# Kernel optimization log

Measured on AMD Instinct MI355X. Metric: run time of the kernel, lower is better.

The kernel has to match this reference:

```python
import jax, jax.numpy as jnp
import numpy as np

G = 64          # groups of the dynamic conv
EPS = 1e-5      # instance-norm epsilon


def setup_inputs() -> dict:
    key = jax.random.key(0)
    ks = jax.random.split(key, 12)
    B, Cin, Cout, S = 16, 512, 256, 512   # batch, in_ch, out_ch, style_dim
    H = W = 32
    cg = Cin // G                          # channels per group (= 8)

    def n(k, shape, scale=0.05):
        return jax.random.normal(k, shape, dtype=jnp.float32) * scale

    return {
        "x": jax.random.normal(ks[0], (B, Cin, H, W), dtype=jnp.float32),
        "w": jax.random.normal(ks[1], (B, S, 3, 3), dtype=jnp.float32),
        # KernelPredictor params
        "kp_sw": n(ks[2], (Cin * cg, S, 3, 3)),   # spatial (depthwise) kernel predictor conv
        "kp_sb": n(ks[3], (Cin * cg,)),
        "kp_pw": n(ks[4], (Cin * cg, S)),          # pointwise kernel predictor (1x1 on pooled style)
        "kp_pb": n(ks[5], (Cin * cg,)),
        "kp_bw": n(ks[6], (Cin, S)),               # bias predictor
        "kp_bb": n(ks[7], (Cin,)),
        # decoder conv stack (convs=2, last changes channels)
        "dec_w1": n(ks[8], (Cin, Cin, 3, 3)),
        "dec_b1": n(ks[9], (Cin,)),
        "dec_w2": n(ks[10], (Cout, Cin, 3, 3)),
        "dec_b2": n(ks[11], (Cout,)),
    }


def _conv(x, w, b=None, groups=1, pad=((1, 1), (1, 1))):
    y = jax.lax.conv_general_dilated(
        x, w, (1, 1), pad, feature_group_count=groups,
        dimension_numbers=("NCHW", "OIHW", "NCHW"))
    if b is not None:
        y = y + b[None, :, None, None]
    return y


def _instance_norm(x):
    m = x.mean(axis=(2, 3), keepdims=True)
    v = x.var(axis=(2, 3), keepdims=True)
    return (x - m) * jax.lax.rsqrt(v + EPS)


def reference(x, w, kp_sw, kp_sb, kp_pw, kp_pb, kp_bw, kp_bb,
              dec_w1, dec_b1, dec_w2, dec_b2):
    B, C, H, W_ = x.shape
    cg = C // G
    # ---- KernelPredictor ----
    # spatial branch: reflect-padded 3x3 conv over the 3x3 style map -> per-sample grouped spatial kernels
    w_pad = jnp.pad(w, ((0, 0), (0, 0), (1, 1), (1, 1)), mode="reflect")
    dw = _conv(w_pad, kp_sw, kp_sb, pad=((0, 0), (0, 0)))      # [B, C*cg, 3, 3]
    dw = dw.reshape(B, C, cg, 3, 3)                             # [B, out, in/g, kh, kw]
    # pointwise + bias branches: global avg pool then 1x1 conv (== matmul)
    pooled = w.mean(axis=(2, 3))                                # [B, S]
    pw = (pooled @ kp_pw.T + kp_pb).reshape(B, G, cg, cg)       # [B, g, out_pg, in_pg]
    bias = pooled @ kp_bw.T + kp_bb                             # [B, C]
    # ---- AdaConv2D: instance-norm, per-sample grouped spatial conv, grouped pointwise conv + bias ----
    xn = _instance_norm(x)
    xp = jnp.pad(xn, ((0, 0), (0, 0), (1, 1), (1, 1)), mode="reflect")

    def per_sample(xi, ki):
        return _conv(xi[None], ki, groups=G, pad=((0, 0), (0, 0)))[0]

    y = jax.vmap(per_sample)(xp, dw)                            # [B, C, H, W]
    yg = y.reshape(B, G, cg, H, W_)
    y = jnp.einsum("bgoi,bgihw->bgohw", pw, yg).reshape(B, C, H, W_)
    y = y + bias[:, :, None, None]
    # ---- decoder conv stack + nearest upsample ----
    y = jax.nn.relu(_conv(y, dec_w1, dec_b1))
    y = jax.nn.relu(_conv(y, dec_w2, dec_b2))
    y = jnp.repeat(jnp.repeat(y, 2, axis=2), 2, axis=3)         # 32x32 -> 64x64 nearest
    return y
```

## Files before the change

kernel.cpp:

```cpp
#include <hip/hip_runtime.h>

using short8 = __attribute__((ext_vector_type(8))) short;
using f32x4  = __attribute__((ext_vector_type(4))) float;

__device__ __forceinline__ unsigned short f2b(float f){
  unsigned int u = __float_as_uint(f);
  u = u + 0x7fffu + ((u >> 16) & 1u);
  return (unsigned short)(u >> 16);
}
__device__ __forceinline__ float b2f(unsigned short s){
  return __uint_as_float(((unsigned int)s) << 16);
}

__device__ __forceinline__ void gll16(const void* g, void* l){
  __builtin_amdgcn_global_load_lds(
      (const __attribute__((address_space(1))) unsigned int*)g,
      (__attribute__((address_space(3))) unsigned int*)l, 16, 0, 0);
}
__device__ __forceinline__ void vm_wait8(){ asm volatile("s_waitcnt vmcnt(8)" ::: "memory"); }
__device__ __forceinline__ void vm_wait4(){ asm volatile("s_waitcnt vmcnt(4)" ::: "memory"); }
__device__ __forceinline__ void vm_wait0(){ asm volatile("s_waitcnt vmcnt(0)" ::: "memory"); }

__global__ __launch_bounds__(256) void k_prepwt(const float* __restrict__ w,
    unsigned short* __restrict__ A, float* __restrict__ pooled,
    const float* __restrict__ w1, const float* __restrict__ w2,
    unsigned short* __restrict__ d1, unsigned short* __restrict__ d2){
  int bid = blockIdx.x;
  if(bid >= 176){
    __shared__ float ld[4608];
    int co = bid - 176;
    const float* src = (co < 512) ? (w1 + (size_t)co * 4608) : (w2 + (size_t)(co - 512) * 4608);
    unsigned short* dst = (co < 512) ? (d1 + (size_t)co * 4608) : (d2 + (size_t)(co - 512) * 4608);
    for(int i = threadIdx.x; i < 4608; i += 256) ld[i] = src[i];
    __syncthreads();
    for(int i = threadIdx.x; i < 4608; i += 256){
      int q = i >> 9, cin = i & 511;
      dst[i] = f2b(ld[cin * 9 + q]);
    }
    return;
  }
  if(bid >= 144){
    int i = (bid - 144) * 256 + threadIdx.x;
    const float* p = w + (size_t)i * 9;
    float s = 0.f;
    #pragma unroll
    for(int j = 0; j < 9; j++) s += p[j];
    pooled[i] = s * (1.f / 9.f);
    return;
  }
  int row = bid;
  int pos = row >> 4, b = row & 15;
  int oh = pos / 3, ow = pos % 3;
  for(int k = threadIdx.x; k < 4608; k += 256){
    int cin = k / 9, q = k - cin * 9;
    int kh = q / 3, kw = q - kh * 3;
    int ih = oh + kh - 1, iw = ow + kw - 1;
    ih = ih < 0 ? -ih : (ih > 2 ? 4 - ih : ih);
    iw = iw < 0 ? -iw : (iw > 2 ? 4 - iw : iw);
    float v = w[((size_t)(b * 512 + cin) * 3 + ih) * 3 + iw];
    A[(size_t)row * 4608 + k] = f2b(v);
  }
}

__global__ __launch_bounds__(256) void k_pwbias(const float* __restrict__ pooled,
    const float* __restrict__ kp_pw, const float* __restrict__ kp_pb,
    const float* __restrict__ kp_bw, const float* __restrict__ kp_bb,
    float* __restrict__ pw, float* __restrict__ bias){
  int wid = (blockIdx.x * 256 + threadIdx.x) >> 6;
  int lane = threadIdx.x & 63;
  const float* row;
  float bv;
  if(wid < 4096){ row = kp_pw + (size_t)wid * 512; bv = kp_pb[wid]; }
  else          { row = kp_bw + (size_t)(wid - 4096) * 512; bv = kp_bb[wid - 4096]; }
  float r[8];
  #pragma unroll
  for(int i = 0; i < 8; i++) r[i] = row[lane + 64 * i];
  for(int b = 0; b < 16; b++){
    float s = 0.f;
    #pragma unroll
    for(int i = 0; i < 8; i++) s += r[i] * pooled[b * 512 + lane + 64 * i];
    #pragma unroll
    for(int o = 32; o >= 1; o >>= 1) s += __shfl_xor(s, o, 64);
    if(lane == 0){
      if(wid < 4096) pw[b * 4096 + wid] = s + bv;
      else           bias[b * 512 + (wid - 4096)] = s + bv;
    }
  }
}

__global__ __launch_bounds__(256) void k_gemmB(const unsigned short* __restrict__ Aim,
    const float* __restrict__ kp_sw, float* __restrict__ part){
  __shared__ unsigned short Al[144 * 72];
  __shared__ unsigned short Bl[64 * 72];
  int tid = threadIdx.x;
  int lane = tid & 63, wv = tid >> 6;
  int n0 = blockIdx.x * 64;
  int kz = blockIdx.y;
  f32x4 acc[9] = {};
  for(int ks = kz * 6; ks < kz * 6 + 6; ks++){
    int kb = ks * 64;
    for(int c = tid; c < 1152; c += 256){
      int m = c >> 3, kc = c & 7;
      *(int4*)&Al[m * 72 + kc * 8] = *(const int4*)(Aim + (size_t)m * 4608 + kb + kc * 8);
    }
    for(int c = tid; c < 512; c += 256){
      int n = c >> 3, kc = c & 7;
      const float4* src = (const float4*)(kp_sw + (size_t)(n0 + n) * 4608 + kb + kc * 8);
      float4 v0 = src[0], v1 = src[1];
      unsigned short tmp[8];
      tmp[0]=f2b(v0.x); tmp[1]=f2b(v0.y); tmp[2]=f2b(v0.z); tmp[3]=f2b(v0.w);
      tmp[4]=f2b(v1.x); tmp[5]=f2b(v1.y); tmp[6]=f2b(v1.z); tmp[7]=f2b(v1.w);
      *(int4*)&Bl[n * 72 + kc * 8] = *(int4*)tmp;
    }
    __syncthreads();
    int r16 = lane & 15, khalf = lane >> 4;
    #pragma unroll
    for(int kk = 0; kk < 2; kk++){
      int ko = kk * 32 + khalf * 8;
      short8 bf = *(const short8*)&Bl[(wv * 16 + r16) * 72 + ko];
      #pragma unroll
      for(int mf = 0; mf < 9; mf++){
        short8 af = *(const short8*)&Al[(mf * 16 + r16) * 72 + ko];
        acc[mf] = __builtin_amdgcn_mfma_f32_16x16x32_bf16(af, bf, acc[mf], 0, 0, 0);
      }
    }
    __syncthreads();
  }
  int r16 = lane & 15, rgrp = lane >> 4;
  int n = n0 + wv * 16 + r16;
  #pragma unroll
  for(int mf = 0; mf < 9; mf++){
    #pragma unroll
    for(int r = 0; r < 4; r++){
      int m = mf * 16 + rgrp * 4 + r;
      part[((size_t)kz * 144 + m) * 4096 + n] = acc[mf][r];
    }
  }
}

__global__ __launch_bounds__(256) void k_red(const float* __restrict__ part,
    const float* __restrict__ kp_sb, float* __restrict__ dw){
  int i = blockIdx.x * 256 + threadIdx.x;
  int m = i >> 12, n = i & 4095;
  float s = kp_sb[n];
  #pragma unroll
  for(int kz = 0; kz < 12; kz++) s += part[((size_t)kz * 144 + m) * 4096 + n];
  int q = m >> 4, b = m & 15;
  dw[((size_t)b * 4096 + n) * 9 + q] = s;
}

__global__ __launch_bounds__(256) void k_ring(unsigned short* __restrict__ y1p){
  int i = blockIdx.x * 256 + threadIdx.x;
  int b = i / 8448, rem = i - b * 8448;
  int e = rem >> 6, ch8 = rem & 63;
  int hh, ww;
  if(e < 34){ hh = 0; ww = e; }
  else if(e < 68){ hh = 33; ww = e - 34; }
  else if(e < 100){ hh = e - 68 + 1; ww = 0; }
  else { hh = e - 100 + 1; ww = 33; }
  int4 z = {0, 0, 0, 0};
  *(int4*)&y1p[((size_t)(b * 34 + hh) * 34 + ww) * 512 + ch8 * 8] = z;
}

__global__ __launch_bounds__(256) void k_ada(const float* __restrict__ x,
    const float* __restrict__ dwb, const float* __restrict__ pwb,
    const float* __restrict__ biasb, unsigned short* __restrict__ y0p){
  __shared__ float xn[8][1156];
  __shared__ float dwl[576];
  __shared__ float pwl[64];
  __shared__ float bl[8];
  __shared__ float red0[4][8], red1[4][8];
  __shared__ float ms[8], rs[8];
  int bg = blockIdx.x; int b = bg >> 6, g = bg & 63;
  int tid = threadIdx.x;
  int lane = tid & 63, wv = tid >> 6;
  for(int i = tid; i < 576; i += 256) dwl[i] = dwb[((size_t)b * 4096 + g * 64) * 9 + i];
  if(tid < 64) pwl[tid] = pwb[b * 4096 + g * 64 + tid];
  if(tid < 8)  bl[tid]  = biasb[b * 512 + g * 8 + tid];
  if(tid < 132){
    int e = tid, hh, ww;
    if(e < 34){ hh = 0; ww = e; }
    else if(e < 68){ hh = 33; ww = e - 34; }
    else if(e < 100){ hh = e - 68 + 1; ww = 0; }
    else { hh = e - 100 + 1; ww = 33; }
    int4 z = {0, 0, 0, 0};
    *(int4*)&y0p[((size_t)(b * 34 + hh) * 34 + ww) * 512 + g * 8] = z;
  }
  const float* xb = x + ((size_t)(b * 512 + g * 8)) * 1024;
  int h4 = tid >> 3, w4 = (tid & 7) * 4;
  float s[8], s2[8];
  #pragma unroll
  for(int ci = 0; ci < 8; ci++){
    float4 v = *(const float4*)(xb + ci * 1024 + tid * 4);
    float* dst = &xn[ci][(h4 + 1) * 34 + w4 + 1];
    dst[0] = v.x; dst[1] = v.y; dst[2] = v.z; dst[3] = v.w;
    s[ci]  = v.x + v.y + v.z + v.w;
    s2[ci] = v.x * v.x + v.y * v.y + v.z * v.z + v.w * v.w;
  }
  #pragma unroll
  for(int ci = 0; ci < 8; ci++){
    #pragma unroll
    for(int o = 32; o >= 1; o >>= 1){
      s[ci]  += __shfl_xor(s[ci],  o, 64);
      s2[ci] += __shfl_xor(s2[ci], o, 64);
    }
  }
  if(lane == 0){
    #pragma unroll
    for(int ci = 0; ci < 8; ci++){ red0[wv][ci] = s[ci]; red1[wv][ci] = s2[ci]; }
  }
  __syncthreads();
  if(tid < 8){
    float S  = red0[0][tid] + red0[1][tid] + red0[2][tid] + red0[3][tid];
    float S2 = red1[0][tid] + red1[1][tid] + red1[2][tid] + red1[3][tid];
    float m = S * (1.f / 1024.f);
    ms[tid] = m;
    rs[tid] = rsqrtf(S2 * (1.f / 1024.f) - m * m + 1e-5f);
  }
  __syncthreads();
  #pragma unroll
  for(int ci = 0; ci < 8; ci++){
    float m = ms[ci], r = rs[ci];
    float* p = &xn[ci][(h4 + 1) * 34 + w4 + 1];
    #pragma unroll
    for(int j = 0; j < 4; j++) p[j] = (p[j] - m) * r;
  }
  __syncthreads();
  for(int idx = tid; idx < 1056; idx += 256){
    int ci = idx / 132, e = idx - ci * 132;
    int hh, ww;
    if(e < 34){ hh = 0; ww = e; }
    else if(e < 68){ hh = 33; ww = e - 34; }
    else if(e < 100){ hh = e - 68 + 1; ww = 0; }
    else { hh = e - 100 + 1; ww = 33; }
    int h = hh - 1, w2 = ww - 1;
    h  = h  < 0 ? 1 : (h  > 31 ? 30 : h);
    w2 = w2 < 0 ? 1 : (w2 > 31 ? 30 : w2);
    xn[ci][hh * 34 + ww] = xn[ci][(h + 1) * 34 + (w2 + 1)];
  }
  __syncthreads();
  float acc[4][8] = {};
  #pragma unroll
  for(int i = 0; i < 8; i++){
    #pragma unroll
    for(int q = 0; q < 9; q++){
      int kh = q / 3, kw = q - kh * 3;
      float dvs[8];
      #pragma unroll
      for(int o = 0; o < 8; o++) dvs[o] = dwl[(o * 8 + i) * 9 + q];
      #pragma unroll
      for(int pp = 0; pp < 4; pp++){
        int p = pp * 256 + tid; int h = p >> 5, w = p & 31;
        float v = xn[i][(h + kh) * 34 + (w + kw)];
        #pragma unroll
        for(int o = 0; o < 8; o++) acc[pp][o] += v * dvs[o];
      }
    }
  }
  #pragma unroll
  for(int pp = 0; pp < 4; pp++){
    int p = pp * 256 + tid; int h = p >> 5, w = p & 31;
    unsigned short pack[8];
    #pragma unroll
    for(int o = 0; o < 8; o++){
      float sv = bl[o];
      #pragma unroll
      for(int i2 = 0; i2 < 8; i2++) sv += pwl[o * 8 + i2] * acc[pp][i2];
      pack[o] = f2b(sv);
    }
    *(int4*)&y0p[((size_t)(b * 34 + h + 1) * 34 + (w + 1)) * 512 + g * 8] = *(int4*)pack;
  }
}

template<int NCOUT, int OUT_PADDED>
__global__ __launch_bounds__(512) void k_conv(const unsigned short* __restrict__ inp,
    const unsigned short* __restrict__ wt, const float* __restrict__ bias,
    unsigned short* __restrict__ outp){
  __shared__ unsigned short Al[4][128 * 64];
  __shared__ unsigned short Bl[4][128 * 64];
  int tid = threadIdx.x;
  int mt = blockIdx.x;
  int n0 = blockIdx.y * 128;
  int b = mt >> 3, h0 = (mt & 7) * 4;
  int lane = tid & 63, wv = tid >> 6;
  int wm = (wv >> 2) * 64, wn = (wv & 3) * 32;
  f32x4 acc[4][2] = {};
  const size_t bbase = (size_t)b * 34 * 34 * 512;

  int kc = tid & 7;
  int m0 = tid >> 3, m1 = (tid + 512) >> 3;
  int colA0 = kc ^ (m0 & 7), colA1 = kc ^ (m1 & 7);
  int mh0 = m0 >> 5, mw0 = m0 & 31;
  int mh1 = m1 >> 5, mw1 = m1 & 31;
  int ldsO0 = (tid & ~63) * 8;
  int ldsO1 = ldsO0 + 512 * 8;
  const unsigned short* a0base = inp + bbase + colA0 * 8;
  const unsigned short* a1base = inp + bbase + colA1 * 8;
  const unsigned short* b0base = wt + (size_t)(n0 + m0) * 4608 + colA0 * 8;
  const unsigned short* b1base = wt + (size_t)(n0 + m1) * 4608 + colA1 * 8;
  int r16 = lane & 15, khalf = lane >> 4;

#define STAGE(T, BUF) { \
    int q_ = (T) >> 3, cb_ = ((T) & 7) * 64; \
    int kh_ = q_ / 3, kw_ = q_ - kh_ * 3; \
    gll16(a0base + (size_t)((h0 + mh0 + kh_) * 34 + mw0 + kw_) * 512 + cb_, &Al[BUF][ldsO0]); \
    gll16(a1base + (size_t)((h0 + mh1 + kh_) * 34 + mw1 + kw_) * 512 + cb_, &Al[BUF][ldsO1]); \
    gll16(b0base + (size_t)q_ * 512 + cb_, &Bl[BUF][ldsO0]); \
    gll16(b1base + (size_t)q_ * 512 + cb_, &Bl[BUF][ldsO1]); }

#define COMPUTE(BUF) { \
    const unsigned short* Ab = Al[BUF]; const unsigned short* Bb = Bl[BUF]; \
    { int sc8 = (khalf ^ (r16 & 7)) * 8; \
      short8 af[4], bf[2]; \
      _Pragma("unroll") for(int i = 0; i < 4; i++) af[i] = *(const short8*)&Ab[(wm + i * 16 + r16) * 64 + sc8]; \
      _Pragma("unroll") for(int i = 0; i < 2; i++) bf[i] = *(const short8*)&Bb[(wn + i * 16 + r16) * 64 + sc8]; \
      __builtin_amdgcn_s_setprio(1); \
      _Pragma("unroll") for(int mi = 0; mi < 4; mi++) \
        _Pragma("unroll") for(int ni = 0; ni < 2; ni++) \
          acc[mi][ni] = __builtin_amdgcn_mfma_f32_16x16x32_bf16(af[mi], bf[ni], acc[mi][ni], 0, 0, 0); \
      __builtin_amdgcn_s_setprio(0); } \
    { int sc8 = ((4 + khalf) ^ (r16 & 7)) * 8; \
      short8 af[4], bf[2]; \
      _Pragma("unroll") for(int i = 0; i < 4; i++) af[i] = *(const short8*)&Ab[(wm + i * 16 + r16) * 64 + sc8]; \
      _Pragma("unroll") for(int i = 0; i < 2; i++) bf[i] = *(const short8*)&Bb[(wn + i * 16 + r16) * 64 + sc8]; \
      __builtin_amdgcn_s_setprio(1); \
      _Pragma("unroll") for(int mi = 0; mi < 4; mi++) \
        _Pragma("unroll") for(int ni = 0; ni < 2; ni++) \
          acc[mi][ni] = __builtin_amdgcn_mfma_f32_16x16x32_bf16(af[mi], bf[ni], acc[mi][ni], 0, 0, 0); \
      __builtin_amdgcn_s_setprio(0); } }

  STAGE(0, 0)
  STAGE(1, 1)
  for(int t = 0; t < 68; t += 4){
    STAGE(t + 2, 2) vm_wait8(); __builtin_amdgcn_s_barrier(); COMPUTE(0)
    STAGE(t + 3, 3) vm_wait8(); __builtin_amdgcn_s_barrier(); COMPUTE(1)
    STAGE(t + 4, 0) vm_wait8(); __builtin_amdgcn_s_barrier(); COMPUTE(2)
    STAGE(t + 5, 1) vm_wait8(); __builtin_amdgcn_s_barrier(); COMPUTE(3)
  }
  STAGE(70, 2) vm_wait8(); __builtin_amdgcn_s_barrier(); COMPUTE(0)
  STAGE(71, 3) vm_wait8(); __builtin_amdgcn_s_barrier(); COMPUTE(1)
  vm_wait4(); __builtin_amdgcn_s_barrier(); COMPUTE(2)
  vm_wait0(); __builtin_amdgcn_s_barrier(); COMPUTE(3)
#undef STAGE
#undef COMPUTE

  int rgrp = lane >> 4;
  #pragma unroll
  for(int ni = 0; ni < 2; ni++){
    int n = n0 + wn + ni * 16 + r16;
    float bv = bias[n];
    #pragma unroll
    for(int mi = 0; mi < 4; mi++){
      #pragma unroll
      for(int r = 0; r < 4; r++){
        int row = wm + mi * 16 + rgrp * 4 + r;
        int h = h0 + (row >> 5), w = row & 31;
        float v = acc[mi][ni][r] + bv;
        v = v > 0.f ? v : 0.f;
        size_t oidx;
        if(OUT_PADDED) oidx = ((size_t)(b * 34 + h + 1) * 34 + (w + 1)) * 512 + n;
        else           oidx = ((size_t)(b * 32 + h) * 32 + w) * NCOUT + n;
        outp[oidx] = f2b(v);
      }
    }
  }
}

__global__ __launch_bounds__(256) void k_up(const unsigned short* __restrict__ y2,
                                            float* __restrict__ out){
  __shared__ unsigned short ld[32 * 258];
  int bh = blockIdx.x; int b = bh >> 5, h = bh & 31;
  int tid = threadIdx.x;
  const unsigned short* src = y2 + ((size_t)b * 1024 + h * 32) * 256;
  for(int c = tid; c < 1024; c += 256){
    int w = c >> 5, kc = c & 31;
    *(int4*)&ld[w * 258 + kc * 8] = *(const int4*)&src[w * 256 + kc * 8];
  }
  __syncthreads();
  int q = tid & 3, co0 = tid >> 2;
  for(int cc = 0; cc < 4; cc++){
    int co = cc * 64 + co0;
    size_t obase = ((size_t)(b * 256 + co) * 64 + h * 2) * 64 + q * 16;
    #pragma unroll
    for(int i = 0; i < 4; i++){
      float a  = b2f(ld[(q * 8 + i * 2) * 258 + co]);
      float b2 = b2f(ld[(q * 8 + i * 2 + 1) * 258 + co]);
      float4 v = make_float4(a, a, b2, b2);
      *(float4*)&out[obase + i * 4]      = v;
      *(float4*)&out[obase + 64 + i * 4] = v;
    }
  }
}

extern "C" void kernel_launch(void* const* d_in, const int* in_sizes, int n_in,
                              void* d_out, int out_size, void* d_ws, size_t ws_size,
                              hipStream_t stream){
  (void)in_sizes; (void)n_in; (void)out_size; (void)ws_size;
  const float* x      = (const float*)d_in[0];
  const float* w      = (const float*)d_in[1];
  const float* kp_sw  = (const float*)d_in[2];
  const float* kp_sb  = (const float*)d_in[3];
  const float* kp_pw  = (const float*)d_in[4];
  const float* kp_pb  = (const float*)d_in[5];
  const float* kp_bw  = (const float*)d_in[6];
  const float* kp_bb  = (const float*)d_in[7];
  const float* dec_w1 = (const float*)d_in[8];
  const float* dec_b1 = (const float*)d_in[9];
  const float* dec_w2 = (const float*)d_in[10];
  const float* dec_b2 = (const float*)d_in[11];
  char* ws = (char*)d_ws;
  float*          pooled = (float*)(ws);
  float*          pw     = (float*)(ws + 32768);
  float*          bias   = (float*)(ws + 294912);
  unsigned short* Aim    = (unsigned short*)(ws + 393216);
  float*          dw     = (float*)(ws + 1720320);
  unsigned short* w1t    = (unsigned short*)(ws + 4079616);
  unsigned short* w2t    = (unsigned short*)(ws + 8798208);
  unsigned short* y0p    = (unsigned short*)(ws + 11157504);
  unsigned short* y1p    = (unsigned short*)(ws + 30097408);
  unsigned short* y2     = (unsigned short*)(ws + 49037312);
  float*          part   = (float*)(ws + 11157504);

  k_prepwt<<<944,  256, 0, stream>>>(w, Aim, pooled, dec_w1, dec_w2, w1t, w2t);
  k_pwbias<<<1152, 256, 0, stream>>>(pooled, kp_pw, kp_pb, kp_bw, kp_bb, pw, bias);
  k_gemmB <<<dim3(64, 12), 256, 0, stream>>>(Aim, kp_sw, part);
  k_red   <<<2304, 256, 0, stream>>>(part, kp_sb, dw);
  k_ring  <<<528,  256, 0, stream>>>(y1p);
  k_ada   <<<1024, 256, 0, stream>>>(x, dw, pw, bias, y0p);
  k_conv<512, 1><<<dim3(128, 4), 512, 0, stream>>>(y0p, w1t, dec_b1, y1p);
  k_conv<256, 0><<<dim3(128, 2), 512, 0, stream>>>(y1p, w2t, dec_b2, y2);
  k_up    <<<512,  256, 0, stream>>>(y2, (float*)d_out);
}
```

Before: 257.4 us.

## Switch conv main loop to double-buffered LDS and fold ring-zeroing into k_ada

The implicit-GEMM conv kernel moves from a 4-stage LDS ring (prefetch distance 2) to a 2-stage double buffer with an extra barrier per step. This halves LDS use from 128KB to 64KB per block, which could allow two 512-thread blocks per CU, but it shortens how far loads are prefetched ahead. Separately, the k_ring zero-border kernel is merged into k_ada as extra blocks, removing one launch.

```diff
diff --git a/kernel.cpp b/kernel.cpp
--- a/kernel.cpp
+++ b/kernel.cpp
@@ -17,7 +17,6 @@
       (const __attribute__((address_space(1))) unsigned int*)g,
       (__attribute__((address_space(3))) unsigned int*)l, 16, 0, 0);
 }
-__device__ __forceinline__ void vm_wait8(){ asm volatile("s_waitcnt vmcnt(8)" ::: "memory"); }
 __device__ __forceinline__ void vm_wait4(){ asm volatile("s_waitcnt vmcnt(4)" ::: "memory"); }
 __device__ __forceinline__ void vm_wait0(){ asm volatile("s_waitcnt vmcnt(0)" ::: "memory"); }
 
@@ -149,29 +148,31 @@
   dw[((size_t)b * 4096 + n) * 9 + q] = s;
 }
 
-__global__ __launch_bounds__(256) void k_ring(unsigned short* __restrict__ y1p){
-  int i = blockIdx.x * 256 + threadIdx.x;
-  int b = i / 8448, rem = i - b * 8448;
-  int e = rem >> 6, ch8 = rem & 63;
-  int hh, ww;
-  if(e < 34){ hh = 0; ww = e; }
-  else if(e < 68){ hh = 33; ww = e - 34; }
-  else if(e < 100){ hh = e - 68 + 1; ww = 0; }
-  else { hh = e - 100 + 1; ww = 33; }
-  int4 z = {0, 0, 0, 0};
-  *(int4*)&y1p[((size_t)(b * 34 + hh) * 34 + ww) * 512 + ch8 * 8] = z;
-}
-
 __global__ __launch_bounds__(256) void k_ada(const float* __restrict__ x,
     const float* __restrict__ dwb, const float* __restrict__ pwb,
-    const float* __restrict__ biasb, unsigned short* __restrict__ y0p){
+    const float* __restrict__ biasb, unsigned short* __restrict__ y0p,
+    unsigned short* __restrict__ y1p){
+  int bg = blockIdx.x;
+  if(bg >= 1024){
+    int i = (bg - 1024) * 256 + threadIdx.x;
+    int b = i / 8448, rem = i - b * 8448;
+    int e = rem >> 6, ch8 = rem & 63;
+    int hh, ww;
+    if(e < 34){ hh = 0; ww = e; }
+    else if(e < 68){ hh = 33; ww = e - 34; }
+    else if(e < 100){ hh = e - 68 + 1; ww = 0; }
+    else { hh = e - 100 + 1; ww = 33; }
+    int4 z = {0, 0, 0, 0};
+    *(int4*)&y1p[((size_t)(b * 34 + hh) * 34 + ww) * 512 + ch8 * 8] = z;
+    return;
+  }
   __shared__ float xn[8][1156];
   __shared__ float dwl[576];
   __shared__ float pwl[64];
   __shared__ float bl[8];
   __shared__ float red0[4][8], red1[4][8];
   __shared__ float ms[8], rs[8];
-  int bg = blockIdx.x; int b = bg >> 6, g = bg & 63;
+  int b = bg >> 6, g = bg & 63;
   int tid = threadIdx.x;
   int lane = tid & 63, wv = tid >> 6;
   for(int i = tid; i < 576; i += 256) dwl[i] = dwb[((size_t)b * 4096 + g * 64) * 9 + i];
@@ -276,8 +277,8 @@
 __global__ __launch_bounds__(512) void k_conv(const unsigned short* __restrict__ inp,
     const unsigned short* __restrict__ wt, const float* __restrict__ bias,
     unsigned short* __restrict__ outp){
-  __shared__ unsigned short Al[4][128 * 64];
-  __shared__ unsigned short Bl[4][128 * 64];
+  __shared__ unsigned short Al[2][128 * 64];
+  __shared__ unsigned short Bl[2][128 * 64];
   int tid = threadIdx.x;
   int mt = blockIdx.x;
   int n0 = blockIdx.y * 128;
@@ -331,16 +332,20 @@
 
   STAGE(0, 0)
   STAGE(1, 1)
-  for(int t = 0; t < 68; t += 4){
-    STAGE(t + 2, 2) vm_wait8(); __builtin_amdgcn_s_barrier(); COMPUTE(0)
-    STAGE(t + 3, 3) vm_wait8(); __builtin_amdgcn_s_barrier(); COMPUTE(1)
-    STAGE(t + 4, 0) vm_wait8(); __builtin_amdgcn_s_barrier(); COMPUTE(2)
-    STAGE(t + 5, 1) vm_wait8(); __builtin_amdgcn_s_barrier(); COMPUTE(3)
-  }
-  STAGE(70, 2) vm_wait8(); __builtin_amdgcn_s_barrier(); COMPUTE(0)
-  STAGE(71, 3) vm_wait8(); __builtin_amdgcn_s_barrier(); COMPUTE(1)
-  vm_wait4(); __builtin_amdgcn_s_barrier(); COMPUTE(2)
-  vm_wait0(); __builtin_amdgcn_s_barrier(); COMPUTE(3)
+  vm_wait4(); __builtin_amdgcn_s_barrier();
+  for(int t = 0; t < 70; t += 2){
+    COMPUTE(0)
+    __builtin_amdgcn_s_barrier();
+    STAGE(t + 2, 0)
+    vm_wait4(); __builtin_amdgcn_s_barrier();
+    COMPUTE(1)
+    __builtin_amdgcn_s_barrier();
+    STAGE(t + 3, 1)
+    vm_wait4(); __builtin_amdgcn_s_barrier();
+  }
+  COMPUTE(0)
+  vm_wait0(); __builtin_amdgcn_s_barrier();
+  COMPUTE(1)
 #undef STAGE
 #undef COMPUTE
 
@@ -425,8 +430,7 @@
   k_pwbias<<<1152, 256, 0, stream>>>(pooled, kp_pw, kp_pb, kp_bw, kp_bb, pw, bias);
   k_gemmB <<<dim3(64, 12), 256, 0, stream>>>(Aim, kp_sw, part);
   k_red   <<<2304, 256, 0, stream>>>(part, kp_sb, dw);
-  k_ring  <<<528,  256, 0, stream>>>(y1p);
-  k_ada   <<<1024, 256, 0, stream>>>(x, dw, pw, bias, y0p);
+  k_ada   <<<1552, 256, 0, stream>>>(x, dw, pw, bias, y0p, y1p);
   k_conv<512, 1><<<dim3(128, 4), 512, 0, stream>>>(y0p, w1t, dec_b1, y1p);
   k_conv<256, 0><<<dim3(128, 2), 512, 0, stream>>>(y1p, w2t, dec_b2, y2);
   k_up    <<<512,  256, 0, stream>>>(y2, (float*)d_out);
```

Measured after the change: 250.7 us. 2.6% less time.
